# Performance work log

Hardware: AMD Instinct MI355X
Metric: run time of the kernel (lower is better)

The kernel has to match this reference:

```python
import jax, jax.numpy as jnp
import numpy as np

IMAGE_SIZE = 320
SIGMA = 0.01      # soft-edge width in NDC units (~1.6 px at 320 res)
CHUNK = 128       # faces per scan step (bounds peak memory)


def setup_inputs() -> dict:
    key = jax.random.key(0)
    k1, k2 = jax.random.split(key)
    verts = jax.random.normal(k1, (4, 778, 3), dtype=jnp.float32) * 0.5
    faces = jax.random.randint(k2, (1538, 3), 0, 778, dtype=jnp.int32)
    return {"verts": verts, "faces": faces}


def _silhouette(verts, faces):
    B = verts.shape[0]
    S = IMAGE_SIZE
    # NMR.forward flips the y axis of verts before rendering
    v = verts * jnp.array([1.0, -1.0, 1.0], dtype=verts.dtype)
    xy = v[..., :2]  # orthographic projection (perspective=False)
    F = faces.shape[0]
    n_chunks = -(-F // CHUNK)
    Fp = n_chunks * CHUNK
    faces_p = jnp.pad(faces, ((0, Fp - F), (0, 0)))
    valid = (jnp.arange(Fp) < F).astype(verts.dtype)
    tri = xy[:, faces_p]  # [B, Fp, 3, 2]
    tri = jnp.moveaxis(tri.reshape(B, n_chunks, CHUNK, 3, 2), 1, 0)  # [nc,B,C,3,2]
    valid = valid.reshape(n_chunks, CHUNK)
    # pixel centers in NDC [-1, 1]
    lin = (jnp.arange(S, dtype=verts.dtype) + 0.5) / S * 2.0 - 1.0
    py, px = jnp.meshgrid(lin, lin, indexing="ij")
    px = px.reshape(-1)  # [P]
    py = py.reshape(-1)

    def edge_d(a, b, sgn):
        # signed distance of every pixel to oriented edge a->b: [B, C, P]
        ex = b[..., 0] - a[..., 0]
        ey = b[..., 1] - a[..., 1]
        inv_len = 1.0 / (jnp.sqrt(ex * ex + ey * ey) + 1e-8)
        d = (ex[..., None] * (py[None, None, :] - a[..., 1:2])
             - ey[..., None] * (px[None, None, :] - a[..., 0:1]))
        return sgn[..., None] * d * inv_len[..., None]

    def body(acc, chunk):
        tri_c, m = chunk  # [B,C,3,2], [C]
        v0, v1, v2 = tri_c[..., 0, :], tri_c[..., 1, :], tri_c[..., 2, :]
        # orientation sign so CW / CCW triangles are handled uniformly
        area2 = ((v1[..., 0] - v0[..., 0]) * (v2[..., 1] - v0[..., 1])
                 - (v1[..., 1] - v0[..., 1]) * (v2[..., 0] - v0[..., 0]))
        sgn = jnp.sign(area2)
        logp = (jax.nn.log_sigmoid(edge_d(v0, v1, sgn) / SIGMA)
                + jax.nn.log_sigmoid(edge_d(v1, v2, sgn) / SIGMA)
                + jax.nn.log_sigmoid(edge_d(v2, v0, sgn) / SIGMA))
        prob = jnp.clip(jnp.exp(logp) * m[None, :, None], 0.0, 1.0 - 1e-6)
        return acc + jnp.sum(jnp.log1p(-prob), axis=1), None

    acc0 = jnp.zeros((B, S * S), dtype=verts.dtype)
    acc, _ = jax.lax.scan(body, acc0, (tri, valid))
    # silhouette = 1 - prod_f (1 - coverage_f), accumulated in log space
    return (1.0 - jnp.exp(acc)).reshape(B, S, S)


def reference(verts, faces):
    return _silhouette(verts, faces)
```

## Files before the change

### kernel.cpp

```cpp
#include <hip/hip_runtime.h>
#include <math.h>


#define IMG_S 320
#define N_FACES 1538
#define N_VERTS 778
#define N_BATCH 4
#define FP 1600
#define TILE 8
#define BLOCK 512
#define CHUNK_F 768
#define NWAVE 8
#define INV_SIGMA 100.0f
#define T_CUT 12.0f
#define ACC_CUT_P 2.2603294e-6f
#define LOG2_1EM6 -19.9315686f

__global__ __launch_bounds__(256)
void prep_faces(const float* __restrict__ verts,
                const int* __restrict__ faces,
                float4* __restrict__ gE0,
                float4* __restrict__ gE1,
                float4* __restrict__ gE2)
{
    const int f = blockIdx.x * 256 + threadIdx.x;
    const int b = blockIdx.z;
    if (f >= N_FACES) return;

    const float* vb = verts + (size_t)b * N_VERTS * 3;
    const int i0 = faces[f * 3 + 0];
    const int i1 = faces[f * 3 + 1];
    const int i2 = faces[f * 3 + 2];
    const float x0 = vb[i0 * 3 + 0], y0 = -vb[i0 * 3 + 1];
    const float x1 = vb[i1 * 3 + 0], y1 = -vb[i1 * 3 + 1];
    const float x2 = vb[i2 * 3 + 0], y2 = -vb[i2 * 3 + 1];

    const float dx1 = x1 - x0, dy1 = y1 - y0;
    const float dx2 = x2 - x0, dy2 = y2 - y0;
    const float area2 = __builtin_fmaf(dx1, dy2, -__fmul_rn(dy1, dx2));
    const float sgn = (area2 > 0.0f) ? 1.0f : ((area2 < 0.0f) ? -1.0f : 0.0f);

    const size_t o = (size_t)b * FP + f;
    {
        const float ex = x1 - x0, ey = y1 - y0;
        const float s = sgn * INV_SIGMA / (sqrtf(ex * ex + ey * ey) + 1e-8f);
        gE0[o] = make_float4(-s * ey, s * ex, s * (ey * x0 - ex * y0), 0.0f);
    }
    {
        const float ex = x2 - x1, ey = y2 - y1;
        const float s = sgn * INV_SIGMA / (sqrtf(ex * ex + ey * ey) + 1e-8f);
        gE1[o] = make_float4(-s * ey, s * ex, s * (ey * x1 - ex * y1), 0.0f);
    }
    {
        const float ex = x0 - x2, ey = y0 - y2;
        const float s = sgn * INV_SIGMA / (sqrtf(ex * ex + ey * ey) + 1e-8f);
        gE2[o] = make_float4(-s * ey, s * ex, s * (ey * x2 - ex * y2), 0.0f);
    }
}

__global__ __launch_bounds__(BLOCK)
void silhouette_ws(const float4* __restrict__ gE0,
                   const float4* __restrict__ gE1,
                   const float4* __restrict__ gE2,
                   float* __restrict__ out)
{
    __shared__ int sIdx[CHUNK_F + 8];
    __shared__ float sAcc[BLOCK];
    __shared__ int sCount;
    __shared__ int sAlive;
    __shared__ int sCover;

    const int t    = threadIdx.x;
    const int wave = t >> 6;
    const int lane = t & 63;
    const int p    = t & 63;
    const int plx  = p & 7;
    const int ply  = p >> 3;
    const int b    = blockIdx.z;
    const int gx   = blockIdx.x * TILE + plx;
    const int gy   = blockIdx.y * TILE + ply;

    const float w  = 2.0f / IMG_S;
    const float px = (gx + 0.5f) * w - 1.0f;
    const float py = (gy + 0.5f) * w - 1.0f;
    const float cx = (blockIdx.x * TILE + 4) * w - 1.0f;
    const float cy = (blockIdx.y * TILE + 4) * w - 1.0f;
    const float rr = 3.5f * w;

    const float4* gb0 = gE0 + (size_t)b * FP;
    const float4* gb1 = gE1 + (size_t)b * FP;
    const float4* gb2 = gE2 + (size_t)b * FP;

    float acc = 1.0f;

    for (int c = 0; c < 2; ++c) {
        const int base = c * CHUNK_F;
        const int end  = (c == 0) ? CHUNK_F : N_FACES;

        sAcc[t] = acc;
        if (t == 0) { sCount = 0; sAlive = 0; sCover = 0; }
        __syncthreads();

        float tot = sAcc[p];
        #pragma unroll
        for (int k = 1; k < NWAVE; ++k) tot *= sAcc[p + 64 * k];
        const bool alive = (tot > ACC_CUT_P);
        if (alive) sAlive = 1;
        __syncthreads();

        if (sAlive == 0) break;

        for (int fb = base; fb < end; fb += BLOCK) {
            const int fc = fb + t;
            const bool vald = (fc < end);
            const int fcc = vald ? fc : (end - 1);
            const float4 e0 = gb0[fcc];
            const float4 e1 = gb1[fcc];
            const float4 e2 = gb2[fcc];
            const float c0 = fmaf(e0.x, cx, fmaf(e0.y, cy, e0.z));
            const float c1 = fmaf(e1.x, cx, fmaf(e1.y, cy, e1.z));
            const float c2 = fmaf(e2.x, cx, fmaf(e2.y, cy, e2.z));
            const float r0 = rr * (fabsf(e0.x) + fabsf(e0.y));
            const float r1 = rr * (fabsf(e1.x) + fabsf(e1.y));
            const float r2 = rr * (fabsf(e2.x) + fabsf(e2.y));
            const float m_hi = fminf(c0 + r0, fminf(c1 + r1, c2 + r2));
            const float m_lo = fminf(c0 - r0, fminf(c1 - r1, c2 - r2));
            const bool isCov  = vald && (m_lo > T_CUT);
            const bool isBand = vald && !isCov && (m_hi > -T_CUT);

            const unsigned long long mb = __ballot(isBand);
            int wbase = 0;
            if (lane == 0) {
                const int nw = __popcll(mb);
                if (nw) wbase = atomicAdd(&sCount, nw);
            }
            wbase = __shfl(wbase, 0);
            if (isBand) {
                sIdx[wbase + __popcll(mb & ((1ull << lane) - 1ull))] = fc;
            }
            const unsigned long long mc = __ballot(isCov);
            if (lane == 0) {
                const int ncv = __popcll(mc);
                if (ncv) atomicAdd(&sCover, ncv);
            }
        }
        __syncthreads();

        const float coverF = exp2f((float)sCover * LOG2_1EM6);
        bool live = alive && (acc * coverF > ACC_CUT_P);
        if (wave == 0) acc *= coverF;

        const int n = sCount;
        int j = wave;
        while (j < n) {
            if (__ballot(live) == 0ull) break;
            const int jstop = j + 4 * NWAVE;
            for (; j < n && j < jstop; j += NWAVE) {
                int fj = sIdx[j];
                fj = __builtin_amdgcn_readfirstlane(fj);
                const float4 e0 = gb0[fj];
                const float4 e1 = gb1[fj];
                const float4 e2 = gb2[fj];
                const float xa = fmaf(e0.x, px, fmaf(e0.y, py, e0.z));
                const float xb = fmaf(e1.x, px, fmaf(e1.y, py, e1.z));
                const float xc = fmaf(e2.x, px, fmaf(e2.y, py, e2.z));
                const float m = fminf(xa, fminf(xb, xc));
                if (live && m > -T_CUT) {
                    float f;
                    if (m > T_CUT) {
                        f = 1e-6f;
                    } else {
                        const float mid = fmaxf(fminf(fmaxf(xa, xb), xc),
                                                fminf(xa, xb));
                        if (mid > T_CUT) {
                            f = 1.0f - __builtin_amdgcn_rcpf(1.0f + __expf(-m));
                        } else {
                            const float da = 1.0f + __expf(-xa);
                            const float db = 1.0f + __expf(-xb);
                            const float dc = 1.0f + __expf(-xc);
                            f = 1.0f - __builtin_amdgcn_rcpf(da * db * dc);
                        }
                    }
                    acc *= f;
                    live = (acc > ACC_CUT_P);
                }
            }
        }

        __syncthreads();
    }

    sAcc[t] = acc;
    __syncthreads();
    if (t < 64) {
        float tot = sAcc[p];
        #pragma unroll
        for (int k = 1; k < NWAVE; ++k) tot *= sAcc[p + 64 * k];
        out[(size_t)b * (IMG_S * IMG_S) + (size_t)gy * IMG_S + gx] = 1.0f - tot;
    }
}

extern "C" void kernel_launch(void* const* d_in, const int* in_sizes, int n_in,
                              void* d_out, int out_size, void* d_ws, size_t ws_size,
                              hipStream_t stream) {
    const float* verts = (const float*)d_in[0];
    const int* faces = (const int*)d_in[1];
    float* out = (float*)d_out;

    float4* gE0 = (float4*)d_ws;
    float4* gE1 = gE0 + (size_t)N_BATCH * FP;
    float4* gE2 = gE1 + (size_t)N_BATCH * FP;

    dim3 pgrid((N_FACES + 255) / 256, 1, N_BATCH);
    prep_faces<<<pgrid, 256, 0, stream>>>(verts, faces, gE0, gE1, gE2);

    dim3 grid(IMG_S / TILE, IMG_S / TILE, N_BATCH);
    silhouette_ws<<<grid, BLOCK, 0, stream>>>(gE0, gE1, gE2, out);
}
```

Measured before the change: 90.51 us.

## Add coarse 32x32 tile classification pass to early-exit saturated and empty tiles

A new kernel classifies each 32x32 pixel super-tile against every face, counting faces that fully cover it and faces whose soft edge band touches it. The main raster kernel reads these counts and immediately writes 1.0 for tiles covered by at least two faces, or 0.0 for tiles that no face reaches, skipping the per-block face scan and the accumulation loop. This adds one extra launch plus a small coarse pass. Skipped covered tiles write exactly 1.0, where the full computation would give a value within float rounding of it.

```diff
diff --git a/kernel.cpp b/kernel.cpp
--- a/kernel.cpp
+++ b/kernel.cpp
@@ -11,6 +11,7 @@
 #define BLOCK 512
 #define CHUNK_F 768
 #define NWAVE 8
+#define CT_PS 10
 #define INV_SIGMA 100.0f
 #define T_CUT 12.0f
 #define ACC_CUT_P 2.2603294e-6f
@@ -58,10 +59,60 @@
     }
 }
 
+__global__ __launch_bounds__(256)
+void prep_coarse(const float4* __restrict__ gE0,
+                 const float4* __restrict__ gE1,
+                 const float4* __restrict__ gE2,
+                 int* __restrict__ gCov,
+                 int* __restrict__ gBand)
+{
+    __shared__ int lCov, lBand;
+    const int t  = threadIdx.x;
+    const int ct = blockIdx.x;
+    const int b  = blockIdx.z;
+    if (t == 0) { lCov = 0; lBand = 0; }
+    __syncthreads();
+
+    const float w  = 2.0f / IMG_S;
+    const float cx = ((ct % CT_PS) * 32 + 16) * w - 1.0f;
+    const float cy = ((ct / CT_PS) * 32 + 16) * w - 1.0f;
+    const float rr = 15.5f * w;
+
+    const float4* gb0 = gE0 + (size_t)b * FP;
+    const float4* gb1 = gE1 + (size_t)b * FP;
+    const float4* gb2 = gE2 + (size_t)b * FP;
+
+    int nc = 0, nb = 0;
+    for (int f = t; f < N_FACES; f += 256) {
+        const float4 e0 = gb0[f];
+        const float4 e1 = gb1[f];
+        const float4 e2 = gb2[f];
+        const float c0 = fmaf(e0.x, cx, fmaf(e0.y, cy, e0.z));
+        const float c1 = fmaf(e1.x, cx, fmaf(e1.y, cy, e1.z));
+        const float c2 = fmaf(e2.x, cx, fmaf(e2.y, cy, e2.z));
+        const float r0 = rr * (fabsf(e0.x) + fabsf(e0.y));
+        const float r1 = rr * (fabsf(e1.x) + fabsf(e1.y));
+        const float r2 = rr * (fabsf(e2.x) + fabsf(e2.y));
+        const float m_hi = fminf(c0 + r0, fminf(c1 + r1, c2 + r2));
+        const float m_lo = fminf(c0 - r0, fminf(c1 - r1, c2 - r2));
+        if (m_lo > T_CUT) nc++;
+        else if (m_hi > -T_CUT) nb++;
+    }
+    atomicAdd(&lCov, nc);
+    atomicAdd(&lBand, nb);
+    __syncthreads();
+    if (t == 0) {
+        gCov[b * (CT_PS * CT_PS) + ct]  = lCov;
+        gBand[b * (CT_PS * CT_PS) + ct] = lBand;
+    }
+}
+
 __global__ __launch_bounds__(BLOCK)
 void silhouette_ws(const float4* __restrict__ gE0,
                    const float4* __restrict__ gE1,
                    const float4* __restrict__ gE2,
+                   const int* __restrict__ gCov,
+                   const int* __restrict__ gBand,
                    float* __restrict__ out)
 {
     __shared__ int sIdx[CHUNK_F + 8];
@@ -79,6 +130,22 @@
     const int b    = blockIdx.z;
     const int gx   = blockIdx.x * TILE + plx;
     const int gy   = blockIdx.y * TILE + ply;
+
+    const int ct   = (blockIdx.y >> 2) * CT_PS + (blockIdx.x >> 2);
+    const int nCov = gCov[b * (CT_PS * CT_PS) + ct];
+    {
+        const int nBnd = gBand[b * (CT_PS * CT_PS) + ct];
+        if (nCov >= 2) {
+            if (t < 64)
+                out[(size_t)b * (IMG_S * IMG_S) + (size_t)gy * IMG_S + gx] = 1.0f;
+            return;
+        }
+        if (nCov == 0 && nBnd == 0) {
+            if (t < 64)
+                out[(size_t)b * (IMG_S * IMG_S) + (size_t)gy * IMG_S + gx] = 0.0f;
+            return;
+        }
+    }
 
     const float w  = 2.0f / IMG_S;
     const float px = (gx + 0.5f) * w - 1.0f;
@@ -210,10 +277,15 @@
     float4* gE0 = (float4*)d_ws;
     float4* gE1 = gE0 + (size_t)N_BATCH * FP;
     float4* gE2 = gE1 + (size_t)N_BATCH * FP;
+    int* gCov  = (int*)(gE2 + (size_t)N_BATCH * FP);
+    int* gBand = gCov + N_BATCH * CT_PS * CT_PS;
 
     dim3 pgrid((N_FACES + 255) / 256, 1, N_BATCH);
     prep_faces<<<pgrid, 256, 0, stream>>>(verts, faces, gE0, gE1, gE2);
 
+    dim3 cgrid(CT_PS * CT_PS, 1, N_BATCH);
+    prep_coarse<<<cgrid, 256, 0, stream>>>(gE0, gE1, gE2, gCov, gBand);
+
     dim3 grid(IMG_S / TILE, IMG_S / TILE, N_BATCH);
-    silhouette_ws<<<grid, BLOCK, 0, stream>>>(gE0, gE1, gE2, out);
-}
+    silhouette_ws<<<grid, BLOCK, 0, stream>>>(gE0, gE1, gE2, gCov, gBand, out);
+}
```

Measured after the change: 93.72 us. 3.5% more time.
